# Optimization experiments

Measured on AMD Instinct MI355X. Metric: run time of the kernel, lower is better.

Reference implementation:

```python
import jax, jax.numpy as jnp
import numpy as np
import math

D_MODEL = 1024

def setup_inputs() -> dict:
    key = jax.random.key(0)
    kx, kq, kk, kv = jax.random.split(key, 4)
    scale = 1.0 / math.sqrt(D_MODEL)
    x = jax.random.normal(kx, (4, 2048, D_MODEL), dtype=jnp.float32)
    W_q = jax.random.normal(kq, (D_MODEL, D_MODEL), dtype=jnp.float32) * scale
    W_k = jax.random.normal(kk, (D_MODEL, D_MODEL), dtype=jnp.float32) * scale
    W_v = jax.random.normal(kv, (D_MODEL, D_MODEL), dtype=jnp.float32) * scale
    return {"x": x, "W_q": W_q, "W_k": W_k, "W_v": W_v}

def reference(x, W_q, W_k, W_v):
    # x: (B, C, d)
    B, C, d = x.shape
    Q = x @ W_q  # (B, C, d)
    K = x @ W_k
    V = x @ W_v
    scores = jnp.einsum('bqd,bkd->bqk', Q, K) / jnp.sqrt(jnp.asarray(d, x.dtype))
    causal = jnp.tril(jnp.ones((C, C), dtype=bool))  # (C, C)
    scores = jnp.where(causal, scores, -jnp.inf)
    attn = jax.nn.softmax(scores, axis=-1)
    return jnp.einsum('bqk,bkd->bqd', attn, V)
```

## Files before the change

### kernel.cpp

```cpp
#include <hip/hip_runtime.h>
#include <hip/hip_bf16.h>


typedef __attribute__((ext_vector_type(8))) __bf16 bf16x8;
typedef __attribute__((ext_vector_type(4))) float f32x4;
typedef __attribute__((ext_vector_type(4))) float float4v;
typedef __attribute__((ext_vector_type(4))) unsigned int uint4v;
typedef __attribute__((ext_vector_type(4))) unsigned short ushort4v;

#define GLL16(gp, lp)                                                        \
  __builtin_amdgcn_global_load_lds(                                          \
      (const __attribute__((address_space(1))) void*)(gp),                   \
      (__attribute__((address_space(3))) void*)(lp), 16, 0, 0)

#define BAR()  __builtin_amdgcn_s_barrier()
#define SB0()  __builtin_amdgcn_sched_barrier(0)
#define WLG0() asm volatile("s_waitcnt lgkmcnt(0)" ::: "memory")
#define WVM4() asm volatile("s_waitcnt vmcnt(4)" ::: "memory")
#define WVM0() asm volatile("s_waitcnt vmcnt(0)" ::: "memory")
#define PRIO(n) __builtin_amdgcn_s_setprio(n)

__device__ __forceinline__ unsigned short f2b(float f) {
  union { float f; unsigned u; } v; v.f = f;
  unsigned r = v.u + 0x7FFF + ((v.u >> 16) & 1);
  return (unsigned short)(r >> 16);
}
__device__ __forceinline__ float b2f(unsigned short h) {
  union { unsigned u; float f; } v; v.u = ((unsigned)h) << 16;
  return v.f;
}
__device__ __forceinline__ void store_out(unsigned short* p, float v) { *p = f2b(v); }
__device__ __forceinline__ void store_out(float* p, float v) { *p = v; }

__global__ __launch_bounds__(256) void k_convert(const float* __restrict__ in,
                                                 unsigned short* __restrict__ out, long n) {
  long i = ((long)blockIdx.x * 256 + threadIdx.x) * 4;
  if (i + 3 < n) {
    float4v v = *reinterpret_cast<const float4v*>(in + i);
    ushort4v o;
    o.x = f2b(v.x); o.y = f2b(v.y); o.z = f2b(v.z); o.w = f2b(v.w);
    *reinterpret_cast<ushort4v*>(out + i) = o;
  }
}

__global__ __launch_bounds__(256) void k_transpose_w(const float* __restrict__ in,
                                                     unsigned short* __restrict__ out) {
  __shared__ float t[32][33];
  int tx = threadIdx.x & 31, ty = threadIdx.x >> 5;
  int c0 = blockIdx.x * 32, r0 = blockIdx.y * 32;
  for (int i = ty; i < 32; i += 8)
    t[i][tx] = in[(long)(r0 + i) * 1024 + c0 + tx];
  __syncthreads();
  for (int i = ty; i < 32; i += 8)
    out[(long)(c0 + i) * 1024 + r0 + tx] = f2b(t[tx][i]);
}

__global__ __launch_bounds__(256) void k_transpose_v(const unsigned short* __restrict__ in,
                                                     unsigned short* __restrict__ out,
                                                     int R, int Cc) {
  __shared__ unsigned short t[32][33];
  long base = (long)blockIdx.z * R * Cc;
  int tx = threadIdx.x & 31, ty = threadIdx.x >> 5;
  int c0 = blockIdx.x * 32, r0 = blockIdx.y * 32;
  for (int i = ty; i < 32; i += 8)
    t[i][tx] = in[base + (long)(r0 + i) * Cc + c0 + tx];
  __syncthreads();
  for (int i = ty; i < 32; i += 8)
    out[base + (long)(c0 + i) * R + r0 + tx] = t[tx][i];
}

#define RDA(buf, half)                                                        \
  _Pragma("unroll") for (int m_ = 0; m_ < 4; ++m_)                            \
  _Pragma("unroll") for (int ks_ = 0; ks_ < 2; ++ks_)                         \
    af[m_][ks_] = *reinterpret_cast<const bf16x8*>(                           \
        (buf) + (arb + (half) * 4 + m_) * 1024 + ks_ * 512 + foff);

#define RDB(buf, half, BF)                                                    \
  _Pragma("unroll") for (int n_ = 0; n_ < 2; ++n_)                            \
  _Pragma("unroll") for (int ks_ = 0; ks_ < 2; ++ks_)                         \
    BF[n_][ks_] = *reinterpret_cast<const bf16x8*>(                           \
        (buf) + (brb + (half) * 2 + n_) * 1024 + ks_ * 512 + foff);

#define QUAD(mh, nh, BF)                                                      \
  _Pragma("unroll") for (int m_ = 0; m_ < 4; ++m_)                            \
  _Pragma("unroll") for (int n_ = 0; n_ < 2; ++n_)                            \
  _Pragma("unroll") for (int ks_ = 0; ks_ < 2; ++ks_)                         \
    acc[(mh) * 4 + m_][(nh) * 2 + n_] =                                       \
        __builtin_amdgcn_mfma_f32_16x16x32_bf16(                              \
            af[m_][ks_], BF[n_][ks_], acc[(mh) * 4 + m_][(nh) * 2 + n_], 0, 0, 0);

#define STGA(buf, h, k0)                                                      \
  GLL16(gA + (long)(128 * (h)) * K + (k0),      (buf) + (16 * (h) + wave) * 512); \
  GLL16(gA + (long)(128 * (h) + 64) * K + (k0), (buf) + (16 * (h) + 8 + wave) * 512);

#define STGB(buf, h, k0)                                                      \
  GLL16(gB + (long)(128 * (h)) * K + (k0),      (buf) + (16 * (h) + wave) * 512); \
  GLL16(gB + (long)(128 * (h) + 64) * K + (k0), (buf) + (16 * (h) + 8 + wave) * 512);

template <typename OutT, bool CAUSAL_SKIP, bool KCAUSAL>
__global__ __launch_bounds__(512, 2) void k_gemm256(
    const unsigned short* __restrict__ A, const unsigned short* __restrict__ Bt,
    OutT* __restrict__ C, int M, int N, int K, float scale,
    long sA, long sB, long sC) {
  constexpr int BM = 256;
  __shared__ __align__(16) unsigned short lds[65536];
  unsigned short* const lA0 = lds;
  unsigned short* const lA1 = lds + 16384;
  unsigned short* const lB0 = lds + 32768;
  unsigned short* const lB1 = lds + 49152;

  const int bm = blockIdx.x, bn = blockIdx.y;
  if (CAUSAL_SKIP && bn > bm) return;
  const long z = blockIdx.z;
  A += z * sA; Bt += z * sB; C += z * sC;

  const int tid = threadIdx.x;
  const int lane = tid & 63, wave = tid >> 6;
  const int row0 = bm * BM, col0 = bn * 256;

  const int kend = KCAUSAL ? min(K, (bm + 1) * BM) : K;
  const int niter = kend >> 7;

  const int scol = ((lane & 3) * 8) ^ ((lane & 32) ? 16 : 0);
  const int srowi = (wave >> 1) * 16 + (lane >> 2);
  const int scolw = (wave & 1) * 32 + scol;
  const unsigned short* gA = A + (long)(row0 + srowi) * K + scolw;
  const unsigned short* gB = Bt + (long)(col0 + srowi) * K + scolw;

  const int foff = ((lane & 15) * 32 + (lane >> 4) * 8) ^ ((lane & 8) ? 16 : 0);
  const int arb = 8 * (wave >> 2);
  const int brb = 4 * (wave & 3);

  bf16x8 af[4][2], bf0[2][2], bf1[2][2];
  f32x4 acc[8][4] = {};

  STGA(lA0, 0, 0); STGA(lA0, 1, 0);
  STGB(lB0, 0, 0); STGB(lB0, 1, 0);
  STGB(lB1, 0, 64); STGA(lA1, 0, 64);
  WVM4();
  BAR(); SB0();

  for (int j = 0; j < niter; ++j) {
    const bool last = (j == niter - 1);
    const int kb = j * 128;
    RDA(lA0, 0); RDB(lB0, 0, bf0);
    STGA(lA1, 1, kb + 64);
    BAR(); WLG0(); SB0();
    PRIO(1); QUAD(0, 0, bf0); PRIO(0);
    BAR(); SB0();
    RDB(lB0, 1, bf1);
    STGB(lB1, 1, kb + 64);
    BAR(); WLG0(); SB0();
    PRIO(1); QUAD(0, 1, bf1); PRIO(0);
    BAR(); SB0();
    RDA(lA0, 1);
    if (!last) { STGB(lB0, 0, kb + 128); }
    BAR(); WLG0(); SB0();
    PRIO(1); QUAD(1, 1, bf1); PRIO(0);
    BAR(); SB0();
    if (!last) { STGA(lA0, 0, kb + 128); }
    BAR();
    if (!last) { WVM4(); } else { WVM0(); }
    SB0();
    PRIO(1); QUAD(1, 0, bf0); PRIO(0);
    BAR(); SB0();
    RDA(lA1, 0); RDB(lB1, 0, bf0);
    if (!last) { STGA(lA0, 1, kb + 128); }
    BAR(); WLG0(); SB0();
    PRIO(1); QUAD(0, 0, bf0); PRIO(0);
    BAR(); SB0();
    RDB(lB1, 1, bf1);
    if (!last) { STGB(lB0, 1, kb + 128); }
    BAR(); WLG0(); SB0();
    PRIO(1); QUAD(0, 1, bf1); PRIO(0);
    BAR(); SB0();
    RDA(lA1, 1);
    if (!last) { STGB(lB1, 0, kb + 192); }
    BAR(); WLG0(); SB0();
    PRIO(1); QUAD(1, 1, bf1); PRIO(0);
    BAR(); SB0();
    if (!last) { STGA(lA1, 0, kb + 192); }
    BAR();
    if (!last) { WVM4(); }
    SB0();
    PRIO(1); QUAD(1, 0, bf0); PRIO(0);
    BAR(); SB0();
  }

  const int or0 = row0 + (wave >> 2) * 128 + (lane >> 4) * 4;
  const int oc0 = col0 + (wave & 3) * 64 + (lane & 15);
#pragma unroll
  for (int mm = 0; mm < 8; ++mm)
#pragma unroll
    for (int nn = 0; nn < 4; ++nn)
#pragma unroll
      for (int jj = 0; jj < 4; ++jj) {
        long idx = (long)(or0 + mm * 16 + jj) * N + (oc0 + nn * 16);
        store_out(&C[idx], acc[mm][nn][jj] * scale);
      }
}

template <typename OutT, bool KCAUSAL, bool REVERSE_X>
__global__ __launch_bounds__(256) void k_gemm128(const unsigned short* __restrict__ A,
                                                 const unsigned short* __restrict__ Bt,
                                                 OutT* __restrict__ C,
                                                 int M, int N, int K, float scale,
                                                 long sA, long sB, long sC) {
  constexpr int BM = 128, BK = 32;
  __shared__ unsigned short As[128 * 32];
  __shared__ unsigned short Bs[128 * 32];
  const int bm = REVERSE_X ? (gridDim.x - 1 - blockIdx.x) : blockIdx.x;
  const int bn = blockIdx.y;
  const long z = blockIdx.z;
  A += z * sA; Bt += z * sB; C += z * sC;

  int tid = threadIdx.x;
  int lane = tid & 63, wave = tid >> 6;
  int wr = (wave >> 1) * 64, wc = (wave & 1) * 64;
  int lr = lane & 15;
  int lk = (lane >> 4) * 8;

  int kend = KCAUSAL ? min(K, (bm + 1) * BM) : K;

  int srow = 32 * wave + (lane >> 2);
  int scol = (lane & 3) * 8;
  const unsigned short* gA = A + (long)(bm * BM + srow) * K + scol;
  const unsigned short* gB = Bt + (long)(bn * 128 + srow) * K + scol;
  const long rowK16 = 16L * (long)K;
  unsigned short* lA = &As[(32 * wave) * 32];
  unsigned short* lB = &Bs[(32 * wave) * 32];

  f32x4 acc[4][4] = {};

  for (int k0 = 0; k0 < kend; k0 += BK) {
    GLL16(gA + k0,          lA);
    GLL16(gA + k0 + rowK16, lA + 16 * 32);
    GLL16(gB + k0,          lB);
    GLL16(gB + k0 + rowK16, lB + 16 * 32);
    __syncthreads();

    bf16x8 af[4], bfr[4];
#pragma unroll
    for (int m = 0; m < 4; ++m)
      af[m] = *reinterpret_cast<const bf16x8*>(&As[(wr + m * 16 + lr) * 32 + lk]);
#pragma unroll
    for (int n = 0; n < 4; ++n)
      bfr[n] = *reinterpret_cast<const bf16x8*>(&Bs[(wc + n * 16 + lr) * 32 + lk]);
#pragma unroll
    for (int m = 0; m < 4; ++m)
#pragma unroll
      for (int n = 0; n < 4; ++n)
        acc[m][n] = __builtin_amdgcn_mfma_f32_16x16x32_bf16(af[m], bfr[n], acc[m][n], 0, 0, 0);
    __syncthreads();
  }

  int orow0 = bm * BM + wr + (lane >> 4) * 4;
  int ocol0 = bn * 128 + wc + lr;
#pragma unroll
  for (int m = 0; m < 4; ++m)
#pragma unroll
    for (int n = 0; n < 4; ++n)
#pragma unroll
      for (int j = 0; j < 4; ++j) {
        long idx = (long)(orow0 + m * 16 + j) * N + (ocol0 + n * 16);
        store_out(&C[idx], acc[m][n][j] * scale);
      }
}

__global__ __launch_bounds__(256) void k_softmax(unsigned short* __restrict__ S, int Cc) {
  long row = blockIdx.x;
  unsigned short* s = S + row * (long)Cc;
  int r = (int)(row & (Cc - 1));
  int n = r + 1;
  int tid = threadIdx.x;
  int lane = tid & 63, wv = tid >> 6;
  int c0 = tid * 8;
  __shared__ float redm[4], reds[4];

  uint4v raw = *reinterpret_cast<const uint4v*>(s + c0);
  float f[8];
#pragma unroll
  for (int i = 0; i < 4; ++i) {
    f[2 * i]     = b2f((unsigned short)(raw[i] & 0xFFFF));
    f[2 * i + 1] = b2f((unsigned short)(raw[i] >> 16));
  }

  float mx = -3.0e38f;
#pragma unroll
  for (int i = 0; i < 8; ++i)
    if (c0 + i < n) mx = fmaxf(mx, f[i]);
#pragma unroll
  for (int o = 32; o > 0; o >>= 1) mx = fmaxf(mx, __shfl_xor(mx, o, 64));
  if (lane == 0) redm[wv] = mx;
  __syncthreads();
  mx = fmaxf(fmaxf(redm[0], redm[1]), fmaxf(redm[2], redm[3]));

  float e[8];
  float sum = 0.f;
#pragma unroll
  for (int i = 0; i < 8; ++i) {
    e[i] = (c0 + i < n) ? __expf(f[i] - mx) : 0.f;
    sum += e[i];
  }
#pragma unroll
  for (int o = 32; o > 0; o >>= 1) sum += __shfl_xor(sum, o, 64);
  if (lane == 0) reds[wv] = sum;
  __syncthreads();
  sum = reds[0] + reds[1] + reds[2] + reds[3];
  float inv = 1.0f / sum;

  uint4v out;
#pragma unroll
  for (int i = 0; i < 4; ++i) {
    unsigned lo = f2b(e[2 * i] * inv);
    unsigned hi = f2b(e[2 * i + 1] * inv);
    out[i] = lo | (hi << 16);
  }
  *reinterpret_cast<uint4v*>(s + c0) = out;
}

extern "C" void kernel_launch(void* const* d_in, const int* in_sizes, int n_in,
                              void* d_out, int out_size, void* d_ws, size_t ws_size,
                              hipStream_t stream) {
  const int B = 4, C = 2048, D = 1024;
  const long MB = (long)B * C;

  const float* x  = (const float*)d_in[0];
  const float* Wq = (const float*)d_in[1];
  const float* Wk = (const float*)d_in[2];
  const float* Wv = (const float*)d_in[3];
  float* out = (float*)d_out;
  char* ws = (char*)d_ws;

  unsigned short* S   = (unsigned short*)(ws);
  unsigned short* Xb  = (unsigned short*)(ws);
  unsigned short* Wt  = (unsigned short*)(ws + 16777216);
  unsigned short* QKV = (unsigned short*)(ws + 33554432);
  unsigned short* Vt  = (unsigned short*)(ws + 83886080);
  unsigned short* Q  = QKV;
  unsigned short* Kk = QKV + MB * D;
  unsigned short* V  = QKV + 2L * MB * D;

  k_convert<<<8192, 256, 0, stream>>>(x, Xb, MB * D);

  dim3 gw(32, 32);
  k_transpose_w<<<gw, 256, 0, stream>>>(Wq, Wt);
  k_transpose_w<<<gw, 256, 0, stream>>>(Wk, Wt + 1048576);
  k_transpose_w<<<gw, 256, 0, stream>>>(Wv, Wt + 2097152);

  k_gemm256<unsigned short, false, false><<<dim3(32, 4, 3), 512, 0, stream>>>(
      Xb, Wt, QKV, (int)MB, D, D, 1.0f, 0L, (long)D * D, MB * D);

  k_transpose_v<<<dim3(32, 64, 4), 256, 0, stream>>>(V, Vt, C, D);

  k_gemm256<unsigned short, true, false><<<dim3(8, 8, 4), 512, 0, stream>>>(
      Q, Kk, S, C, C, D, 1.0f / 32.0f, (long)C * D, (long)C * D, (long)C * C);

  k_softmax<<<B * C, 256, 0, stream>>>(S, C);

  k_gemm128<float, true, true><<<dim3(16, 8, 4), 256, 0, stream>>>(
      S, Vt, out, C, D, C, 1.0f, (long)C * C, (long)D * C, (long)C * D);
}
```

Before: 268.9 us.

## Skip masked causal score tiles, vectorize V transpose, fuse weight transposes

Switches the QK^T score GEMM to the 128-tile kernel with early exit for blocks entirely above the causal diagonal. Softmax now only reads and writes columns up to the end of the current 128-wide key tile. The V transpose uses 64x64 tiles with 4-wide vector accesses, and the three weight transposes are merged into one launch. This is meant to cut the wasted compute and memory traffic on masked regions, though the smaller GEMM tile may be less efficient per flop than the 256 kernel.

```diff
diff --git a/kernel.cpp b/kernel.cpp
--- a/kernel.cpp
+++ b/kernel.cpp
@@ -43,30 +43,45 @@
   }
 }
 
-__global__ __launch_bounds__(256) void k_transpose_w(const float* __restrict__ in,
-                                                     unsigned short* __restrict__ out) {
+__global__ __launch_bounds__(256) void k_transpose_w3(const float* __restrict__ Wq,
+                                                      const float* __restrict__ Wk,
+                                                      const float* __restrict__ Wv,
+                                                      unsigned short* __restrict__ out) {
   __shared__ float t[32][33];
+  const float* in = blockIdx.z == 0 ? Wq : (blockIdx.z == 1 ? Wk : Wv);
+  unsigned short* o = out + (long)blockIdx.z * 1048576;
   int tx = threadIdx.x & 31, ty = threadIdx.x >> 5;
   int c0 = blockIdx.x * 32, r0 = blockIdx.y * 32;
   for (int i = ty; i < 32; i += 8)
     t[i][tx] = in[(long)(r0 + i) * 1024 + c0 + tx];
   __syncthreads();
   for (int i = ty; i < 32; i += 8)
-    out[(long)(c0 + i) * 1024 + r0 + tx] = f2b(t[tx][i]);
+    o[(long)(c0 + i) * 1024 + r0 + tx] = f2b(t[tx][i]);
 }
 
 __global__ __launch_bounds__(256) void k_transpose_v(const unsigned short* __restrict__ in,
                                                      unsigned short* __restrict__ out,
                                                      int R, int Cc) {
-  __shared__ unsigned short t[32][33];
-  long base = (long)blockIdx.z * R * Cc;
-  int tx = threadIdx.x & 31, ty = threadIdx.x >> 5;
-  int c0 = blockIdx.x * 32, r0 = blockIdx.y * 32;
-  for (int i = ty; i < 32; i += 8)
-    t[i][tx] = in[base + (long)(r0 + i) * Cc + c0 + tx];
+  __shared__ unsigned short t[64][68];
+  long base = (long)blockIdx.z * (long)R * Cc;
+  int c0 = blockIdx.x * 64, r0 = blockIdx.y * 64;
+  int tid = threadIdx.x;
+  int a = tid >> 4;
+  int g4 = (tid & 15) * 4;
+#pragma unroll
+  for (int it = 0; it < 4; ++it) {
+    int i = a + it * 16;
+    *reinterpret_cast<ushort4v*>(&t[i][g4]) =
+        *reinterpret_cast<const ushort4v*>(&in[base + (long)(r0 + i) * Cc + c0 + g4]);
+  }
   __syncthreads();
-  for (int i = ty; i < 32; i += 8)
-    out[base + (long)(c0 + i) * R + r0 + tx] = t[tx][i];
+#pragma unroll
+  for (int it = 0; it < 4; ++it) {
+    int c = a + it * 16;
+    ushort4v v;
+    v.x = t[g4 + 0][c]; v.y = t[g4 + 1][c]; v.z = t[g4 + 2][c]; v.w = t[g4 + 3][c];
+    *reinterpret_cast<ushort4v*>(&out[base + (long)(c0 + c) * R + r0 + g4]) = v;
+  }
 }
 
 #define RDA(buf, half)                                                        \
@@ -200,7 +215,7 @@
       }
 }
 
-template <typename OutT, bool KCAUSAL, bool REVERSE_X>
+template <typename OutT, bool CAUSAL_SKIP, bool KCAUSAL, bool REVERSE_X>
 __global__ __launch_bounds__(256) void k_gemm128(const unsigned short* __restrict__ A,
                                                  const unsigned short* __restrict__ Bt,
                                                  OutT* __restrict__ C,
@@ -211,6 +226,7 @@
   __shared__ unsigned short Bs[128 * 32];
   const int bm = REVERSE_X ? (gridDim.x - 1 - blockIdx.x) : blockIdx.x;
   const int bn = blockIdx.y;
+  if (CAUSAL_SKIP && bn > bm) return;
   const long z = blockIdx.z;
   A += z * sA; Bt += z * sB; C += z * sC;
 
@@ -272,12 +288,15 @@
   unsigned short* s = S + row * (long)Cc;
   int r = (int)(row & (Cc - 1));
   int n = r + 1;
+  int ktile = (r | 127) + 1;
   int tid = threadIdx.x;
   int lane = tid & 63, wv = tid >> 6;
   int c0 = tid * 8;
+  bool act = c0 < ktile;
   __shared__ float redm[4], reds[4];
 
-  uint4v raw = *reinterpret_cast<const uint4v*>(s + c0);
+  uint4v raw = {0, 0, 0, 0};
+  if (act) raw = *reinterpret_cast<const uint4v*>(s + c0);
   float f[8];
 #pragma unroll
   for (int i = 0; i < 4; ++i) {
@@ -309,14 +328,16 @@
   sum = reds[0] + reds[1] + reds[2] + reds[3];
   float inv = 1.0f / sum;
 
-  uint4v out;
-#pragma unroll
-  for (int i = 0; i < 4; ++i) {
-    unsigned lo = f2b(e[2 * i] * inv);
-    unsigned hi = f2b(e[2 * i + 1] * inv);
-    out[i] = lo | (hi << 16);
-  }
-  *reinterpret_cast<uint4v*>(s + c0) = out;
+  if (act) {
+    uint4v out;
+#pragma unroll
+    for (int i = 0; i < 4; ++i) {
+      unsigned lo = f2b(e[2 * i] * inv);
+      unsigned hi = f2b(e[2 * i + 1] * inv);
+      out[i] = lo | (hi << 16);
+    }
+    *reinterpret_cast<uint4v*>(s + c0) = out;
+  }
 }
 
 extern "C" void kernel_launch(void* const* d_in, const int* in_sizes, int n_in,
@@ -343,21 +364,18 @@
 
   k_convert<<<8192, 256, 0, stream>>>(x, Xb, MB * D);
 
-  dim3 gw(32, 32);
-  k_transpose_w<<<gw, 256, 0, stream>>>(Wq, Wt);
-  k_transpose_w<<<gw, 256, 0, stream>>>(Wk, Wt + 1048576);
-  k_transpose_w<<<gw, 256, 0, stream>>>(Wv, Wt + 2097152);
+  k_transpose_w3<<<dim3(32, 32, 3), 256, 0, stream>>>(Wq, Wk, Wv, Wt);
 
   k_gemm256<unsigned short, false, false><<<dim3(32, 4, 3), 512, 0, stream>>>(
       Xb, Wt, QKV, (int)MB, D, D, 1.0f, 0L, (long)D * D, MB * D);
 
-  k_transpose_v<<<dim3(32, 64, 4), 256, 0, stream>>>(V, Vt, C, D);
-
-  k_gemm256<unsigned short, true, false><<<dim3(8, 8, 4), 512, 0, stream>>>(
+  k_transpose_v<<<dim3(16, 32, 4), 256, 0, stream>>>(V, Vt, C, D);
+
+  k_gemm128<unsigned short, true, false, false><<<dim3(16, 16, 4), 256, 0, stream>>>(
       Q, Kk, S, C, C, D, 1.0f / 32.0f, (long)C * D, (long)C * D, (long)C * C);
 
   k_softmax<<<B * C, 256, 0, stream>>>(S, C);
 
-  k_gemm128<float, true, true><<<dim3(16, 8, 4), 256, 0, stream>>>(
+  k_gemm128<float, false, true, true><<<dim3(16, 8, 4), 256, 0, stream>>>(
       S, Vt, out, C, D, C, 1.0f, (long)C * C, (long)D * C, (long)C * D);
 }
```

New measurement: 284.3 us. +5.7%, slower.
